# Kernel optimization log

Measured on AMD Instinct MI355X. Metric: run time of the kernel, lower is better.

The kernel has to match this reference:

```python
import jax, jax.numpy as jnp
import numpy as np

B, DIM, H = 64, 768, 12
WH, WW = 14, 14
N = WH * WW + 1  # 197
HD = DIM // H    # 64
NUM_REL = (2 * WH - 1) * (2 * WW - 1) + 3  # 732


def _relative_position_index(wh, ww):
    coords = np.stack(np.meshgrid(np.arange(wh), np.arange(ww), indexing='ij'))  # [2,wh,ww]
    flat = coords.reshape(2, -1)                                                # [2, wh*ww]
    rel = flat[:, :, None] - flat[:, None, :]                                   # [2, M, M]
    rel = rel.transpose(1, 2, 0).astype(np.int64)                               # [M, M, 2]
    rel[:, :, 0] += wh - 1
    rel[:, :, 1] += ww - 1
    rel[:, :, 0] *= 2 * ww - 1
    nrd = (2 * wh - 1) * (2 * ww - 1) + 3
    m = wh * ww
    idx = np.zeros((m + 1, m + 1), dtype=np.int32)
    idx[1:, 1:] = rel.sum(-1)
    idx[0, :] = nrd - 3
    idx[:, 0] = nrd - 2
    idx[0, 0] = nrd - 1
    return idx


def setup_inputs() -> dict:
    key = jax.random.key(0)
    ks = jax.random.split(key, 7)
    x = jax.random.normal(ks[0], (B, N, DIM), dtype=jnp.float32)
    Wqkv = jax.random.normal(ks[1], (3 * DIM, DIM), dtype=jnp.float32) * 0.02
    q_bias = jax.random.normal(ks[2], (DIM,), dtype=jnp.float32) * 0.02
    v_bias = jax.random.normal(ks[3], (DIM,), dtype=jnp.float32) * 0.02
    rel_table = jax.random.normal(ks[4], (NUM_REL, H), dtype=jnp.float32) * 0.02
    Wproj = jax.random.normal(ks[5], (DIM, DIM), dtype=jnp.float32) * 0.02
    bproj = jax.random.normal(ks[6], (DIM,), dtype=jnp.float32) * 0.02
    rel_index = jnp.asarray(_relative_position_index(WH, WW))  # [N, N] int32
    return {"x": x, "Wqkv": Wqkv, "q_bias": q_bias, "v_bias": v_bias,
            "rel_table": rel_table, "Wproj": Wproj, "bproj": bproj,
            "rel_index": rel_index}


def reference(x, Wqkv, q_bias, v_bias, rel_table, Wproj, bproj, rel_index):
    b, n, c = x.shape
    hd = Wqkv.shape[0] // (3 * H)
    scale = hd ** -0.5
    qkv_bias = jnp.concatenate([q_bias, jnp.zeros_like(v_bias), v_bias])
    qkv = x @ Wqkv.T + qkv_bias                              # [B,N,3*DIM]
    qkv = qkv.reshape(b, n, 3, H, hd).transpose(2, 0, 3, 1, 4)  # [3,B,H,N,hd]
    q, k, v = qkv[0] * scale, qkv[1], qkv[2]
    attn = jnp.einsum('bhqd,bhkd->bhqk', q, k)               # [B,H,N,N]
    rel_bias = rel_table[rel_index].transpose(2, 0, 1)       # [H,N,N]
    attn = jax.nn.softmax(attn + rel_bias[None], axis=-1)
    out = jnp.einsum('bhqk,bhkd->bhqd', attn, v)             # [B,H,N,hd]
    out = out.transpose(0, 2, 1, 3).reshape(b, n, -1)        # [B,N,DIM]
    return out @ Wproj.T + bproj
```

## Files before the change

kernel.cpp:

```cpp
#include <hip/hip_runtime.h>

typedef _Float16 f16_t;
typedef f16_t f16x8 __attribute__((ext_vector_type(8)));
typedef float f32x4 __attribute__((ext_vector_type(4)));

#define DEVI __device__ __forceinline__

constexpr int NB    = 64;
constexpr int NTOK  = 197;
constexpr int NH    = 12;
constexpr int DIM   = 768;
constexpr int M_TOK = NB * NTOK;
constexpr int NPAD  = 224;
constexpr float SCALE = 0.125f;

constexpr int KP_SZ  = 2 * NPAD * 32;
constexpr int VTS_SZ = 7 * 64 * 32;
constexpr int P_LD   = 228;
constexpr int PW_SZ  = 16 * P_LD;
constexpr int ATTN_LDS = (KP_SZ + VTS_SZ + 8 * PW_SZ) * 2;

DEVI ushort f2h_bits(float f) { _Float16 h = (_Float16)f; return __builtin_bit_cast(ushort, h); }

DEVI void gload16(const void* g, void* l) {
    __builtin_amdgcn_global_load_lds((const __attribute__((address_space(1))) void*)g,
                                     (__attribute__((address_space(3))) void*)l, 16, 0, 0);
}

__global__ __launch_bounds__(256) void k_cvt(const float* __restrict__ in, ushort* __restrict__ out, int n4) {
    int i = blockIdx.x * 256 + threadIdx.x;
    if (i >= n4) return;
    float4 v = reinterpret_cast<const float4*>(in)[i];
    ushort4 o;
    o.x = f2h_bits(v.x); o.y = f2h_bits(v.y); o.z = f2h_bits(v.z); o.w = f2h_bits(v.w);
    reinterpret_cast<ushort4*>(out)[i] = o;
}

__global__ __launch_bounds__(256) void k_bias(const float* __restrict__ rel_table,
                                              const int* __restrict__ rel_index,
                                              ushort* __restrict__ biash) {
    int idx = blockIdx.x * 256 + threadIdx.x;
    if (idx >= NH * NPAD * 256) return;
    const int j  = idx & 15;
    const int fr = (idx >> 4) & 15;
    const int i  = (idx >> 8) % NPAD;
    const int h  = (idx >> 8) / NPAD;
    const int col = j * 16 + fr;
    float v = -30000.f;
    if (i < NTOK && col < NTOK && j < 14) v = rel_table[rel_index[i * NTOK + col] * NH + h];
    biash[idx] = f2h_bits(v);
}

__global__ __launch_bounds__(512, 2) void k_qkv8(const ushort* __restrict__ A, const ushort* __restrict__ BT,
                                                 const float* __restrict__ b_q, const float* __restrict__ b_v,
                                                 ushort* __restrict__ outp) {
    constexpr int M = M_TOK, N = 2304, K = 768, nt = K / 64;
    extern __shared__ ushort lds[];
    ushort* ldsA = lds;
    ushort* ldsB = lds + 32768;
    const int tid = threadIdx.x, wid = tid >> 6, lane = tid & 63;
    const int wm = wid >> 2, wn = wid & 3;
    const int fr = lane & 15, fg = lane >> 4;
    const int m0 = blockIdx.y * 256, n0 = blockIdx.x * 256;

    const int srow = tid >> 2;
    const int sc = ((tid & 3) ^ ((tid >> 3) & 3)) * 8;
    int ra0 = m0 + srow;       ra0 = ra0 < M ? ra0 : M - 1;
    int ra1 = m0 + srow + 128; ra1 = ra1 < M ? ra1 : M - 1;
    const ushort* pA0 = A + (size_t)ra0 * K + sc;
    const ushort* pA1 = A + (size_t)ra1 * K + sc;
    const ushort* pB0 = BT + (size_t)(n0 + srow) * K + sc;
    const ushort* pB1 = BT + (size_t)(n0 + srow + 128) * K + sc;
    const int dstt = tid * 8;

    int aoff[8], boff[4];
#pragma unroll
    for (int mi = 0; mi < 8; ++mi) {
        const int r = wm * 128 + mi * 16 + fr;
        aoff[mi] = r * 32 + ((fg ^ ((r >> 1) & 3)) * 8);
    }
#pragma unroll
    for (int j = 0; j < 4; ++j) {
        const int c = wn * 64 + j * 16 + fr;
        boff[j] = c * 32 + ((fg ^ ((c >> 1) & 3)) * 8);
    }

    f32x4 acc[8][4] = {};
    f16x8 av[8];

    auto STAGE = [&](int T, int isA, int k) {
        const int Tw = T >= nt ? T - nt : T;
        const size_t so = (size_t)(Tw * 64 + k * 32);
        const int db = (T & 1) * 16384 + k * 8192 + dstt;
        if (isA) { gload16(pA0 + so, ldsA + db); gload16(pA1 + so, ldsA + db + 4096); }
        else     { gload16(pB0 + so, ldsB + db); gload16(pB1 + so, ldsB + db + 4096); }
    };

#define LDA8(B_, KS_) { _Pragma("unroll") for (int mi = 0; mi < 8; ++mi) \
        av[mi] = *(const f16x8*)(ldsA + (B_) * 16384 + (KS_) * 8192 + aoff[mi]); }

#define PHASE(B_, KS_, NH_, LA_, ST_T, ST_A, ST_K, GATE_) { \
        if (LA_) LDA8(B_, KS_); \
        f16x8 bv0 = *(const f16x8*)(ldsB + (B_) * 16384 + (KS_) * 8192 + boff[(NH_) * 2]); \
        f16x8 bv1 = *(const f16x8*)(ldsB + (B_) * 16384 + (KS_) * 8192 + boff[(NH_) * 2 + 1]); \
        STAGE(ST_T, ST_A, ST_K); \
        __builtin_amdgcn_s_barrier(); \
        __builtin_amdgcn_s_setprio(1); \
        _Pragma("unroll") for (int mi = 0; mi < 8; ++mi) { \
            acc[mi][(NH_) * 2]     = __builtin_amdgcn_mfma_f32_16x16x32_f16(av[mi], bv0, acc[mi][(NH_) * 2], 0, 0, 0); \
            acc[mi][(NH_) * 2 + 1] = __builtin_amdgcn_mfma_f32_16x16x32_f16(av[mi], bv1, acc[mi][(NH_) * 2 + 1], 0, 0, 0); } \
        __builtin_amdgcn_s_setprio(0); \
        asm volatile("s_waitcnt lgkmcnt(0)" ::: "memory"); \
        __builtin_amdgcn_sched_barrier(0); \
        if (GATE_) { asm volatile("s_waitcnt vmcnt(4)" ::: "memory"); __builtin_amdgcn_sched_barrier(0); } \
        __builtin_amdgcn_s_barrier(); }

    STAGE(0, 1, 0); STAGE(0, 0, 0); STAGE(0, 1, 1); STAGE(0, 0, 1);
    STAGE(1, 1, 0); STAGE(1, 0, 0);
    asm volatile("s_waitcnt vmcnt(4)" ::: "memory");
    __builtin_amdgcn_sched_barrier(0);
    __builtin_amdgcn_s_barrier();

    for (int i = 0; i < nt / 2; ++i) {
        const int t0 = 2 * i;
        PHASE(0, 0, 0, 1, t0 + 1, 1, 1, 0)
        PHASE(0, 0, 1, 0, t0 + 1, 0, 1, 0)
        PHASE(0, 1, 0, 1, t0 + 2, 1, 0, 0)
        PHASE(0, 1, 1, 0, t0 + 2, 0, 0, 1)
        PHASE(1, 0, 0, 1, t0 + 2, 1, 1, 0)
        PHASE(1, 0, 1, 0, t0 + 2, 0, 1, 0)
        PHASE(1, 1, 0, 1, t0 + 3, 1, 0, 0)
        PHASE(1, 1, 1, 0, t0 + 3, 0, 0, 1)
    }
#undef PHASE
#undef LDA8

    asm volatile("s_waitcnt vmcnt(0) lgkmcnt(0)" ::: "memory");
    __builtin_amdgcn_sched_barrier(0);
    __builtin_amdgcn_s_barrier();

    ushort* ws = lds + wid * 8192;
#pragma unroll
    for (int ni = 0; ni < 4; ++ni) {
        const int col = n0 + wn * 64 + ni * 16 + fr;
        float addv, mul;
        if (col < 768)       { addv = b_q[col]; mul = SCALE; }
        else if (col < 1536) { addv = 0.f; mul = 1.f; }
        else                 { addv = b_v[col - 1536]; mul = 1.f; }
#pragma unroll
        for (int mi = 0; mi < 8; ++mi)
#pragma unroll
            for (int r = 0; r < 4; ++r)
                ws[(mi * 16 + fg * 4 + r) * 64 + ni * 16 + fr] = f2h_bits((acc[mi][ni][r] + addv) * mul);
    }
    __syncthreads();
#pragma unroll
    for (int it = 0; it < 16; ++it) {
        const int g = it * 64 + lane;
        const int r = g >> 3, seg = g & 7;
        const int row = m0 + wm * 128 + r;
        uint4 v = *(const uint4*)(ws + r * 64 + seg * 8);
        if (row < M) *(uint4*)(outp + (size_t)row * N + n0 + wn * 64 + seg * 8) = v;
    }
}

template<int EPI>
__global__ __launch_bounds__(256) void k_gemm(const ushort* __restrict__ A, const ushort* __restrict__ BT,
                                              int M, int N, int K,
                                              const float* __restrict__ b_q, const float* __restrict__ b_v,
                                              const float* __restrict__ b_p,
                                              ushort* __restrict__ out_h, float* __restrict__ out_f) {
    __shared__ __align__(16) ushort lds[2][8192];
    const int tid = threadIdx.x, wid = tid >> 6, lane = tid & 63;
    const int wm = wid >> 1, wn = wid & 1;
    const int fr = lane & 15, fg = lane >> 4;
    const int m0 = blockIdx.y * 128, n0 = blockIdx.x * 128;

    int rA[2], rB[2], cs[2], dst[2];
#pragma unroll
    for (int i = 0; i < 2; ++i) {
        const int g = (wid * 2 + i) * 64 + lane;
        const int row = g >> 2, sp = g & 3;
        cs[i]  = (sp ^ ((row >> 1) & 3)) * 8;
        dst[i] = (wid * 2 + i) * 512;
        const int ra = m0 + row;
        rA[i] = ra < M ? ra : M - 1;
        rB[i] = n0 + row;
    }

    f32x4 acc[4][4] = {};
    const int nt = K / 32;

    auto stage = [&](int t, int buf) {
#pragma unroll
        for (int i = 0; i < 2; ++i)
            gload16(A + (size_t)rA[i] * K + t * 32 + cs[i], &lds[buf][dst[i]]);
#pragma unroll
        for (int i = 0; i < 2; ++i)
            gload16(BT + (size_t)rB[i] * K + t * 32 + cs[i], &lds[buf][4096 + dst[i]]);
    };

    stage(0, 0);
    __syncthreads();
    for (int t = 0; t < nt; ++t) {
        const int cur = t & 1;
        if (t + 1 < nt) stage(t + 1, cur ^ 1);
        const ushort* As = lds[cur];
        const ushort* Bs = lds[cur] + 4096;
        f16x8 af[4], bf[4];
#pragma unroll
        for (int i = 0; i < 4; ++i) {
            const int r = wm * 64 + i * 16 + fr;
            af[i] = *(const f16x8*)(As + r * 32 + ((fg ^ ((r >> 1) & 3)) * 8));
        }
#pragma unroll
        for (int i = 0; i < 4; ++i) {
            const int c = wn * 64 + i * 16 + fr;
            bf[i] = *(const f16x8*)(Bs + c * 32 + ((fg ^ ((c >> 1) & 3)) * 8));
        }
#pragma unroll
        for (int mi = 0; mi < 4; ++mi)
#pragma unroll
            for (int ni = 0; ni < 4; ++ni)
                acc[mi][ni] = __builtin_amdgcn_mfma_f32_16x16x32_f16(af[mi], bf[ni], acc[mi][ni], 0, 0, 0);
        __syncthreads();
    }

#pragma unroll
    for (int ni = 0; ni < 4; ++ni) {
        const int col = n0 + wn * 64 + ni * 16 + fr;
        float addv = 0.f, mul = 1.f;
        if (EPI == 0) {
            if (col < 768)       { addv = b_q[col]; mul = SCALE; }
            else if (col < 1536) { addv = 0.f; }
            else                 { addv = b_v[col - 1536]; }
        } else {
            addv = b_p[col];
        }
#pragma unroll
        for (int mi = 0; mi < 4; ++mi) {
#pragma unroll
            for (int r = 0; r < 4; ++r) {
                const int row = m0 + wm * 64 + mi * 16 + fg * 4 + r;
                if (row < M) {
                    float v = (acc[mi][ni][r] + addv) * mul;
                    if (EPI == 0) out_h[(size_t)row * N + col] = f2h_bits(v);
                    else          out_f[(size_t)row * N + col] = v;
                }
            }
        }
    }
}

__global__ __launch_bounds__(512) void k_attn(const ushort* __restrict__ qkv,
                                              const ushort* __restrict__ biash, ushort* __restrict__ out) {
    extern __shared__ ushort sm[];
    ushort* kp  = sm;
    ushort* vts = sm + KP_SZ;
    ushort* ps  = sm + KP_SZ + VTS_SZ;
    const int tid = threadIdx.x, wid = tid >> 6, lane = tid & 63;
    const int fr = lane & 15, fg = lane >> 4;
    const int bh = blockIdx.x;
    const int b = bh / NH, h = bh % NH;
    const size_t qb = (size_t)(b * NTOK) * 2304;
    const int swz8 = (fg ^ ((fr >> 1) & 3)) * 8;

    ushort* vtile = ps;
    for (int t = tid; t < NPAD * 8; t += 512) {
        const int row = t >> 3, seg = t & 7;
        uint4 kv = make_uint4(0u, 0u, 0u, 0u), vv = make_uint4(0u, 0u, 0u, 0u);
        if (row < NTOK) {
            const ushort* src = qkv + qb + (size_t)row * 2304 + 768 + h * 64;
            kv = *reinterpret_cast<const uint4*>(src + seg * 8);
            vv = *reinterpret_cast<const uint4*>(src + 768 + seg * 8);
        }
        const int pcg = (seg & 3) ^ ((row >> 1) & 3);
        *reinterpret_cast<uint4*>(kp + (seg >> 2) * (NPAD * 32) + row * 32 + pcg * 8) = kv;
        *reinterpret_cast<uint4*>(vtile + row * 72 + seg * 8) = vv;
    }
    __syncthreads();
    for (int o = tid; o < 7 * 64 * 4; o += 512) {
        const int kc = o >> 8, rem = o & 255, d = rem >> 2, pcg = rem & 3;
        const int k0 = kc * 32 + (pcg ^ ((d >> 1) & 3)) * 8;
        ushort w[8];
#pragma unroll
        for (int e = 0; e < 8; ++e) w[e] = vtile[(k0 + e) * 72 + d];
        uint4 val;
        val.x = (uint)w[0] | ((uint)w[1] << 16);
        val.y = (uint)w[2] | ((uint)w[3] << 16);
        val.z = (uint)w[4] | ((uint)w[5] << 16);
        val.w = (uint)w[6] | ((uint)w[7] << 16);
        *reinterpret_cast<uint4*>(vts + kc * 2048 + d * 32 + pcg * 8) = val;
    }
    __syncthreads();

    ushort* pw = ps + wid * PW_SZ;

    for (int s = wid; s < 13; s += 8) {
        const int q0 = s * 16;
        f16x8 qf[2];
        {
            int row = q0 + fr;
            row = row < NTOK ? row : NTOK - 1;
            const ushort* qp = qkv + qb + (size_t)row * 2304 + h * 64 + fg * 8;
            qf[0] = *reinterpret_cast<const f16x8*>(qp);
            qf[1] = *reinterpret_cast<const f16x8*>(qp + 32);
        }
        f32x4 sacc[14] = {};
#pragma unroll
        for (int j = 0; j < 14; ++j) {
#pragma unroll
            for (int kh = 0; kh < 2; ++kh) {
                f16x8 kf = *reinterpret_cast<const f16x8*>(kp + kh * (NPAD * 32) + (j * 16 + fr) * 32 + swz8);
                sacc[j] = __builtin_amdgcn_mfma_f32_16x16x32_f16(qf[kh], kf, sacc[j], 0, 0, 0);
            }
        }
        float rs4[4];
#pragma unroll
        for (int r = 0; r < 4; ++r) {
            const int qrow_l = fg * 4 + r;
            int qrow = q0 + qrow_l;
            qrow = qrow < NTOK ? qrow : NTOK - 1;
            const ushort* bp16 = biash + (((size_t)(h * NPAD + qrow) * 16 + fr) << 4);
            f16x8 bv0 = *reinterpret_cast<const f16x8*>(bp16);
            f16x8 bv1 = *reinterpret_cast<const f16x8*>(bp16 + 8);
            float mx = -1e30f;
#pragma unroll
            for (int j = 0; j < 14; ++j) {
                const float bj = (float)(j < 8 ? bv0[j] : bv1[j - 8]);
                float v = sacc[j][r] + bj;
                sacc[j][r] = v;
                mx = fmaxf(mx, v);
            }
            mx = fmaxf(mx, __shfl_xor(mx, 1));
            mx = fmaxf(mx, __shfl_xor(mx, 2));
            mx = fmaxf(mx, __shfl_xor(mx, 4));
            mx = fmaxf(mx, __shfl_xor(mx, 8));
            float sum = 0.f;
            ushort* prow = pw + qrow_l * P_LD;
#pragma unroll
            for (int j = 0; j < 14; ++j) {
                float p = __expf(sacc[j][r] - mx);
                sum += p;
                prow[j * 16 + fr] = f2h_bits(p);
            }
            sum += __shfl_xor(sum, 1);
            sum += __shfl_xor(sum, 2);
            sum += __shfl_xor(sum, 4);
            sum += __shfl_xor(sum, 8);
            rs4[r] = sum;
        }
        f32x4 o[4] = {};
#pragma unroll
        for (int kc = 0; kc < 7; ++kc) {
            f16x8 af = *reinterpret_cast<const f16x8*>(pw + fr * P_LD + kc * 32 + fg * 8);
#pragma unroll
            for (int dt = 0; dt < 4; ++dt) {
                f16x8 bv = *reinterpret_cast<const f16x8*>(vts + kc * 2048 + (dt * 16 + fr) * 32 + swz8);
                o[dt] = __builtin_amdgcn_mfma_f32_16x16x32_f16(af, bv, o[dt], 0, 0, 0);
            }
        }
#pragma unroll
        for (int dt = 0; dt < 4; ++dt) {
#pragma unroll
            for (int r = 0; r < 4; ++r) {
                const int qrow = q0 + fg * 4 + r;
                if (qrow < NTOK) {
                    const float val = o[dt][r] / rs4[r];
                    out[(size_t)(b * NTOK + qrow) * DIM + h * 64 + dt * 16 + fr] = f2h_bits(val);
                }
            }
        }
    }
}

extern "C" void kernel_launch(void* const* d_in, const int* in_sizes, int n_in,
                              void* d_out, int out_size, void* d_ws, size_t ws_size,
                              hipStream_t stream) {
    const float* x         = (const float*)d_in[0];
    const float* Wqkv      = (const float*)d_in[1];
    const float* q_bias    = (const float*)d_in[2];
    const float* v_bias    = (const float*)d_in[3];
    const float* rel_table = (const float*)d_in[4];
    const float* Wproj     = (const float*)d_in[5];
    const float* bproj     = (const float*)d_in[6];
    const int*   rel_index = (const int*)d_in[7];
    float* out = (float*)d_out;

    char* p = (char*)d_ws;
    auto alloc = [&](size_t bytes) { char* r = p; p += (bytes + 255) & ~(size_t)255; return r; };
    ushort* xb     = (ushort*)alloc((size_t)M_TOK * DIM * 2);
    ushort* wqkvb  = (ushort*)alloc((size_t)2304 * 768 * 2);
    ushort* wprojb = (ushort*)alloc((size_t)768 * 768 * 2);
    ushort* qkvb   = (ushort*)alloc((size_t)M_TOK * 2304 * 2);
    ushort* biasb  = (ushort*)alloc((size_t)NH * NPAD * 256 * 2);
    ushort* aob    = (ushort*)alloc((size_t)M_TOK * DIM * 2);

    (void)hipFuncSetAttribute((const void*)k_qkv8, hipFuncAttributeMaxDynamicSharedMemorySize, 131072);
    (void)hipFuncSetAttribute((const void*)k_attn, hipFuncAttributeMaxDynamicSharedMemorySize, ATTN_LDS);

    int n4 = M_TOK * DIM / 4;
    k_cvt<<<(n4 + 255) / 256, 256, 0, stream>>>(x, xb, n4);
    n4 = 2304 * 768 / 4;
    k_cvt<<<(n4 + 255) / 256, 256, 0, stream>>>(Wqkv, wqkvb, n4);
    n4 = 768 * 768 / 4;
    k_cvt<<<(n4 + 255) / 256, 256, 0, stream>>>(Wproj, wprojb, n4);
    int nbias = NH * NPAD * 256;
    k_bias<<<(nbias + 255) / 256, 256, 0, stream>>>(rel_table, rel_index, biasb);

    k_qkv8<<<dim3(2304 / 256, (M_TOK + 255) / 256), 512, 131072, stream>>>(
        xb, wqkvb, q_bias, v_bias, qkvb);
    k_attn<<<dim3(NB * NH), 512, ATTN_LDS, stream>>>(qkvb, biasb, aob);
    k_gemm<1><<<dim3(768 / 128, (M_TOK + 127) / 128), 256, 0, stream>>>(
        aob, wprojb, M_TOK, 768, 768, nullptr, nullptr, bproj, nullptr, out);
}
```

Measured before the change: 166.0 us.

## Add XCD-aware block swizzle to GEMMs and merge conversion kernels

Remaps GEMM workgroup IDs so that consecutive tiles land on the same XCD. Neighbouring tiles that share A/B panels then hit the same L2. The three fp32-to-fp16 conversion launches are also merged into one kernel that does a ranged dispatch, which saves two launches. The swizzle adds a little index arithmetic, and the merged kernel adds a branch per thread.

```diff
diff --git a/kernel.cpp b/kernel.cpp
--- a/kernel.cpp
+++ b/kernel.cpp
@@ -27,13 +27,24 @@
                                      (__attribute__((address_space(3))) void*)l, 16, 0, 0);
 }
 
-__global__ __launch_bounds__(256) void k_cvt(const float* __restrict__ in, ushort* __restrict__ out, int n4) {
+DEVI int xcd_swz(int orig, int nwg) {
+    const int q = nwg >> 3, r = nwg & 7;
+    const int xcd = orig & 7, idx = orig >> 3;
+    return (xcd < r ? xcd * (q + 1) : r * (q + 1) + (xcd - r) * q) + idx;
+}
+
+__global__ __launch_bounds__(256) void k_cvt3(const float* __restrict__ s0, ushort* __restrict__ d0, int n0,
+                                              const float* __restrict__ s1, ushort* __restrict__ d1, int n1,
+                                              const float* __restrict__ s2, ushort* __restrict__ d2, int n2) {
     int i = blockIdx.x * 256 + threadIdx.x;
-    if (i >= n4) return;
-    float4 v = reinterpret_cast<const float4*>(in)[i];
+    const float* s; ushort* d;
+    if (i < n0)           { s = s0; d = d0; }
+    else if (i < n0 + n1) { i -= n0; s = s1; d = d1; }
+    else                  { i -= n0 + n1; if (i >= n2) return; s = s2; d = d2; }
+    float4 v = reinterpret_cast<const float4*>(s)[i];
     ushort4 o;
     o.x = f2h_bits(v.x); o.y = f2h_bits(v.y); o.z = f2h_bits(v.z); o.w = f2h_bits(v.w);
-    reinterpret_cast<ushort4*>(out)[i] = o;
+    reinterpret_cast<ushort4*>(d)[i] = o;
 }
 
 __global__ __launch_bounds__(256) void k_bias(const float* __restrict__ rel_table,
@@ -55,13 +66,15 @@
                                                  const float* __restrict__ b_q, const float* __restrict__ b_v,
                                                  ushort* __restrict__ outp) {
     constexpr int M = M_TOK, N = 2304, K = 768, nt = K / 64;
+    constexpr int NWG = (N / 256) * 50;
     extern __shared__ ushort lds[];
     ushort* ldsA = lds;
     ushort* ldsB = lds + 32768;
     const int tid = threadIdx.x, wid = tid >> 6, lane = tid & 63;
     const int wm = wid >> 2, wn = wid & 3;
     const int fr = lane & 15, fg = lane >> 4;
-    const int m0 = blockIdx.y * 256, n0 = blockIdx.x * 256;
+    const int bid = xcd_swz(blockIdx.y * (N / 256) + blockIdx.x, NWG);
+    const int m0 = (bid / (N / 256)) * 256, n0 = (bid % (N / 256)) * 256;
 
     const int srow = tid >> 2;
     const int sc = ((tid & 3) ^ ((tid >> 3) & 3)) * 8;
@@ -166,7 +179,7 @@
 
 template<int EPI>
 __global__ __launch_bounds__(256) void k_gemm(const ushort* __restrict__ A, const ushort* __restrict__ BT,
-                                              int M, int N, int K,
+                                              int M, int N, int K, int nwg,
                                               const float* __restrict__ b_q, const float* __restrict__ b_v,
                                               const float* __restrict__ b_p,
                                               ushort* __restrict__ out_h, float* __restrict__ out_f) {
@@ -174,7 +187,9 @@
     const int tid = threadIdx.x, wid = tid >> 6, lane = tid & 63;
     const int wm = wid >> 1, wn = wid & 1;
     const int fr = lane & 15, fg = lane >> 4;
-    const int m0 = blockIdx.y * 128, n0 = blockIdx.x * 128;
+    const int nbx = N / 128;
+    const int bid = xcd_swz(blockIdx.y * nbx + blockIdx.x, nwg);
+    const int m0 = (bid / nbx) * 128, n0 = (bid % nbx) * 128;
 
     int rA[2], rB[2], cs[2], dst[2];
 #pragma unroll
@@ -399,12 +414,8 @@
     (void)hipFuncSetAttribute((const void*)k_qkv8, hipFuncAttributeMaxDynamicSharedMemorySize, 131072);
     (void)hipFuncSetAttribute((const void*)k_attn, hipFuncAttributeMaxDynamicSharedMemorySize, ATTN_LDS);
 
-    int n4 = M_TOK * DIM / 4;
-    k_cvt<<<(n4 + 255) / 256, 256, 0, stream>>>(x, xb, n4);
-    n4 = 2304 * 768 / 4;
-    k_cvt<<<(n4 + 255) / 256, 256, 0, stream>>>(Wqkv, wqkvb, n4);
-    n4 = 768 * 768 / 4;
-    k_cvt<<<(n4 + 255) / 256, 256, 0, stream>>>(Wproj, wprojb, n4);
+    const int n0 = M_TOK * DIM / 4, n1 = 2304 * 768 / 4, n2 = 768 * 768 / 4;
+    k_cvt3<<<(n0 + n1 + n2 + 255) / 256, 256, 0, stream>>>(x, xb, n0, Wqkv, wqkvb, n1, Wproj, wprojb, n2);
     int nbias = NH * NPAD * 256;
     k_bias<<<(nbias + 255) / 256, 256, 0, stream>>>(rel_table, rel_index, biasb);
 
@@ -412,5 +423,6 @@
         xb, wqkvb, q_bias, v_bias, qkvb);
     k_attn<<<dim3(NB * NH), 512, ATTN_LDS, stream>>>(qkvb, biasb, aob);
     k_gemm<1><<<dim3(768 / 128, (M_TOK + 127) / 128), 256, 0, stream>>>(
-        aob, wprojb, M_TOK, 768, 768, nullptr, nullptr, bproj, nullptr, out);
-}
+        aob, wprojb, M_TOK, 768, 768, (768 / 128) * ((M_TOK + 127) / 128),
+        nullptr, nullptr, bproj, nullptr, out);
+}
```

After: 154.3 us. 1.08x faster.
